# Kernel optimization log

Hardware: AMD Instinct MI355X
Metric: run time of the kernel (lower is better)

Reference implementation:

```python
import jax, jax.numpy as jnp
import numpy as np

T, N, F = 8, 4096, 256  # timesteps, nodes, feature dim (in=out for both layers)


def _uniform(key, shape, fan):
    s = 1.0 / np.sqrt(fan)
    return jax.random.uniform(key, shape, jnp.float32, -s, s)


def setup_inputs() -> dict:
    key = jax.random.key(0)
    ks = jax.random.split(key, 32)
    inp = {}
    # dense stand-in for the normalized sparse adjacency Ahat, per timestep
    inp["A"] = jax.random.normal(ks[0], (T, N, N), jnp.float32) * 0.01
    inp["X"] = jax.random.normal(ks[1], (T, N, F), jnp.float32)
    inp["mask"] = jnp.zeros((T, N), jnp.int32)  # only mask.shape[0] is used
    i = 2
    for l in range(2):
        inp[f"l{l}_scorer"] = _uniform(ks[i], (F, 1), F); i += 1
        for g in ("z", "r", "h"):
            inp[f"l{l}_W{g}"] = _uniform(ks[i], (F, F), F); i += 1
            inp[f"l{l}_U{g}"] = _uniform(ks[i], (F, F), F); i += 1
            inp[f"l{l}_b{g}"] = jnp.zeros((F, F), jnp.float32)
        inp[f"l{l}_Q0"] = _uniform(ks[i], (F, F), F); i += 1  # GCN_init_weights
    return inp


def _run_layer(A, Xseq, scorer, Wz, Uz, bz, Wr, Ur, br, Wh, Uh, bh, Q0):
    sn = jnp.linalg.norm(scorer)
    k = Q0.shape[1]  # cols = out_feats

    def step(Q, xs):
        Ahat, embs = xs  # [N,N], [N,F]
        # TopK module: scale rows by tanh(score), take first k rows, transpose -> [F, k]
        scores = (embs @ scorer) / sn            # [N,1]
        zt = (embs * jnp.tanh(scores))[:k].T     # [F, k]
        # matrix GRU evolving the GCN weight matrix Q [F, k]
        upd = jax.nn.sigmoid(Wz @ zt + Uz @ Q + bz)
        rst = jax.nn.sigmoid(Wr @ zt + Ur @ Q + br)
        hcap = jnp.tanh(Wh @ zt + Uh @ (rst * Q) + bh)
        Qn = (1.0 - upd) * Q + upd * hcap
        # GCN step: relu(Ahat @ (embs @ Qn))
        out = jax.nn.relu(Ahat @ (embs @ Qn))    # [N, k]
        return Qn, out

    _, outs = jax.lax.scan(step, Q0, (A, Xseq))
    return outs  # [T, N, k]


def reference(A, X, mask,
              l0_scorer, l0_Wz, l0_Uz, l0_bz, l0_Wr, l0_Ur, l0_br, l0_Wh, l0_Uh, l0_bh, l0_Q0,
              l1_scorer, l1_Wz, l1_Uz, l1_bz, l1_Wr, l1_Ur, l1_br, l1_Wh, l1_Uh, l1_bh, l1_Q0):
    h1 = _run_layer(A, X, l0_scorer, l0_Wz, l0_Uz, l0_bz, l0_Wr, l0_Ur, l0_br, l0_Wh, l0_Uh, l0_bh, l0_Q0)
    h2 = _run_layer(A, h1, l1_scorer, l1_Wz, l1_Uz, l1_bz, l1_Wr, l1_Ur, l1_br, l1_Wh, l1_Uh, l1_bh, l1_Q0)
    return h2[-1]  # [N, F] (skipfeats=False)
```

## Files before the change

kernel.cpp:

```cpp
#include <hip/hip_runtime.h>
#include <math.h>


typedef unsigned short u16;
typedef __attribute__((ext_vector_type(8))) short bhalf8;
typedef __attribute__((ext_vector_type(16))) float f32x16;

__device__ __forceinline__ void split2(float f, unsigned &h, unsigned &l){
  unsigned u = __float_as_uint(f);
  h = u >> 16;
  float r = f - __uint_as_float(u & 0xFFFF0000u);
  l = __float_as_uint(r) >> 16;
}

__launch_bounds__(256)
__global__ void prep_kernel(const float* __restrict__ q0, const float* __restrict__ q1,
                            const float* __restrict__ sc0, const float* __restrict__ sc1,
                            float* __restrict__ q0a, float* __restrict__ q1a,
                            float* __restrict__ sn){
  int b = blockIdx.x, tid = threadIdx.x;
  if (b < 256){ q0a[b*256 + tid] = q0[b*256 + tid]; }
  else if (b < 512){ int r = b - 256; q1a[r*256 + tid] = q1[r*256 + tid]; }
  else {
    __shared__ float s0[256], s1[256];
    float a = sc0[tid]; float c = sc1[tid];
    s0[tid] = a*a; s1[tid] = c*c; __syncthreads();
    for (int off = 128; off > 0; off >>= 1){
      if (tid < off){ s0[tid] += s0[tid+off]; s1[tid] += s1[tid+off]; }
      __syncthreads();
    }
    if (tid == 0){ sn[0] = sqrtf(s0[0]); sn[1] = sqrtf(s1[0]); }
  }
}

__launch_bounds__(256)
__global__ void scores_kernel(const float* __restrict__ emb, long embStrideT,
                              const float* __restrict__ scorer,
                              const float* __restrict__ sn, int snIdx,
                              float* __restrict__ ts, int tsStrideT){
  int t = blockIdx.y;
  int wave = threadIdx.x >> 6, lane = threadIdx.x & 63;
  int j = blockIdx.x*4 + wave;
  const float* row = emb + (long)t*embStrideT + (long)j*256;
  float s = 0.f;
  for (int c = lane; c < 256; c += 64) s += row[c] * scorer[c];
  for (int off = 32; off > 0; off >>= 1) s += __shfl_down(s, off);
  if (lane == 0) ts[t*tsStrideT + j] = tanhf(s / sn[snIdx]);
}

__launch_bounds__(256)
__global__ void split_kernel(const float* __restrict__ src, long sStride,
                             u16* __restrict__ dh, u16* __restrict__ dl,
                             long dStride, int n8){
  int z = blockIdx.y;
  const float* S = src + (long)z * sStride;
  u16* H = dh + (long)z * dStride;
  u16* L = dl + (long)z * dStride;
  int i = blockIdx.x * 256 + threadIdx.x;
  if (i >= n8) return;
  long o = (long)i * 8;
  float4 v0 = *(const float4*)(S + o);
  float4 v1 = *(const float4*)(S + o + 4);
  unsigned h0,h1,h2,h3,h4,h5,h6,h7, l0,l1,l2,l3,l4,l5,l6,l7;
  split2(v0.x,h0,l0); split2(v0.y,h1,l1); split2(v0.z,h2,l2); split2(v0.w,h3,l3);
  split2(v1.x,h4,l4); split2(v1.y,h5,l5); split2(v1.z,h6,l6); split2(v1.w,h7,l7);
  uint4 ph, pl;
  ph.x = h0 | (h1<<16); ph.y = h2 | (h3<<16); ph.z = h4 | (h5<<16); ph.w = h6 | (h7<<16);
  pl.x = l0 | (l1<<16); pl.y = l2 | (l3<<16); pl.z = l4 | (l5<<16); pl.w = l6 | (l7<<16);
  *(uint4*)(H + o) = ph;
  *(uint4*)(L + o) = pl;
}

__launch_bounds__(256)
__global__ void tconv_kernel(const float* __restrict__ src, long sStride,
                             u16* __restrict__ dh, u16* __restrict__ dl, long dStride){
  int z = blockIdx.z;
  const float* S = src + (long)z * sStride;
  u16* H = dh + (long)z * dStride;
  u16* L = dl + (long)z * dStride;
  int k0 = blockIdx.x << 5, n0 = blockIdx.y << 5;
  int c = threadIdx.x & 31, r = threadIdx.x >> 5;
  __shared__ float s[32][33];
  #pragma unroll
  for (int i = 0; i < 4; i++)
    s[r + 8*i][c] = S[(long)(k0 + r + 8*i) * 256 + n0 + c];
  __syncthreads();
  #pragma unroll
  for (int i = 0; i < 4; i++){
    int rr = r + 8*i;
    unsigned h, l;
    split2(s[c][rr], h, l);
    H[(long)(n0 + rr) * 4096 + k0 + c] = (u16)h;
    L[(long)(n0 + rr) * 4096 + k0 + c] = (u16)l;
  }
}

__device__ __forceinline__ int swzA(int row, int kb){
  return (row << 7) + (kb ^ ((row & 7) << 4));
}

__launch_bounds__(256, 2)
// ... 81 lines not shown
  float* po = pout + (long)(m0 + wm) * 256 + (n0 + wn);
  int rb16 = lhi << 2;
  #pragma unroll
  for (int reg = 0; reg < 16; reg++){
    int r = (reg & 3) + ((reg >> 2) << 3) + rb16;
    po[(long)r * 256 + ln31]              = acc00[reg];
    po[(long)r * 256 + 32 + ln31]         = acc01[reg];
    po[(long)(r + 32) * 256 + ln31]       = acc10[reg];
    po[(long)(r + 32) * 256 + 32 + ln31]  = acc11[reg];
  }
}

__launch_bounds__(256)
__global__ void reduce4_kernel(const float* __restrict__ P, long zStrideP, long ksStride,
                               float* __restrict__ out, long zStrideO, int count4, int relu){
  int z = blockIdx.y;
  const float* p = P + (long)z * zStrideP;
  float* o = out + (long)z * zStrideO;
  int i = blockIdx.x * 256 + threadIdx.x;
  if (i >= count4) return;
  long b = (long)i * 4;
  float4 v0 = *(const float4*)(p + b);
  float4 v1 = *(const float4*)(p + ksStride + b);
  float4 v2 = *(const float4*)(p + 2*ksStride + b);
  float4 v3 = *(const float4*)(p + 3*ksStride + b);
  float4 r;
  r.x = v0.x+v1.x+v2.x+v3.x; r.y = v0.y+v1.y+v2.y+v3.y;
  r.z = v0.z+v1.z+v2.z+v3.z; r.w = v0.w+v1.w+v2.w+v3.w;
  if (relu){ r.x=fmaxf(r.x,0.f); r.y=fmaxf(r.y,0.f); r.z=fmaxf(r.z,0.f); r.w=fmaxf(r.w,0.f); }
  *(float4*)(o + b) = r;
}

__launch_bounds__(256)
__global__ void gates_kernel(const float* __restrict__ emb,
                             const float* __restrict__ Wz, const float* __restrict__ Wr, const float* __restrict__ Wh,
                             const float* __restrict__ Uz, const float* __restrict__ Ur,
                             const float* __restrict__ bz, const float* __restrict__ br,
                             const float* __restrict__ Qcur, const float* __restrict__ ts,
                             float* __restrict__ G){
  int bx = blockIdx.x;
  int g = bx >> 6, tile = bx & 63;
  int m0 = (tile >> 3) << 5, j0 = (tile & 7) << 5;
  const float* W = (g==0) ? Wz : (g==1) ? Wr : Wh;
  int tid = threadIdx.x, tx = tid & 15, ty = tid >> 4;
  int rs = tid >> 3, cs = (tid & 7) << 2;
  __shared__ float sA[32][33];
  __shared__ float sB[32][33];
  float a00=0,a01=0,a10=0,a11=0;
  for (int k0 = 0; k0 < 256; k0 += 32){
    const float* pw = W   + (m0+rs)*256 + k0 + cs;
    const float* pe = emb + (long)(j0+rs)*256 + k0 + cs;
    sA[rs][cs+0]=pw[0]; sA[rs][cs+1]=pw[1]; sA[rs][cs+2]=pw[2]; sA[rs][cs+3]=pw[3];
    sB[cs+0][rs]=pe[0]; sB[cs+1][rs]=pe[1]; sB[cs+2][rs]=pe[2]; sB[cs+3][rs]=pe[3];
    __syncthreads();
    #pragma unroll
    for (int k = 0; k < 32; k++){
      float x0=sA[ty][k], x1=sA[ty+16][k], y0=sB[k][tx], y1=sB[k][tx+16];
      a00 += x0*y0; a01 += x0*y1; a10 += x1*y0; a11 += x1*y1;
    }
    __syncthreads();
  }
  float t0 = ts[j0+tx], t1 = ts[j0+tx+16];
  a00*=t0; a10*=t0; a01*=t1; a11*=t1;
  if (g == 2){
    G[2*65536 + (m0+ty   )*256 + j0+tx   ] = a00;
    G[2*65536 + (m0+ty   )*256 + j0+tx+16] = a01;
    G[2*65536 + (m0+ty+16)*256 + j0+tx   ] = a10;
    G[2*65536 + (m0+ty+16)*256 + j0+tx+16] = a11;
    return;
  }
  const float* U  = (g==0) ? Uz : Ur;
  const float* bb = (g==0) ? bz : br;
  float u00=0,u01=0,u10=0,u11=0;
  for (int k0 = 0; k0 < 256; k0 += 32){
    const float* pu = U    + (m0+rs)*256 + k0 + cs;
    const float* pq = Qcur + (k0+rs)*256 + j0 + cs;
    sA[rs][cs+0]=pu[0]; sA[rs][cs+1]=pu[1]; sA[rs][cs+2]=pu[2]; sA[rs][cs+3]=pu[3];
    sB[rs][cs+0]=pq[0]; sB[rs][cs+1]=pq[1]; sB[rs][cs+2]=pq[2]; sB[rs][cs+3]=pq[3];
    __syncthreads();
    #pragma unroll
    for (int k = 0; k < 32; k++){
      float x0=sA[ty][k], x1=sA[ty+16][k], y0=sB[k][tx], y1=sB[k][tx+16];
      u00 += x0*y0; u01 += x0*y1; u10 += x1*y0; u11 += x1*y1;
    }
    __syncthreads();
  }
  int m = m0+ty, j = j0+tx;
  float v;
  v = a00+u00+bb[m*256+j];          G[g*65536 + m*256+j]          = 1.f/(1.f+__expf(-v));
  v = a01+u01+bb[m*256+j+16];       G[g*65536 + m*256+j+16]       = 1.f/(1.f+__expf(-v));
  v = a10+u10+bb[(m+16)*256+j];     G[g*65536 + (m+16)*256+j]     = 1.f/(1.f+__expf(-v));
  v = a11+u11+bb[(m+16)*256+j+16];  G[g*65536 + (m+16)*256+j+16]  = 1.f/(1.f+__expf(-v));
}

__launch_bounds__(256)
__global__ void update_kernel(const float* __restrict__ Uh, const float* __restrict__ bh,
                              const float* __restrict__ G, const float* __restrict__ Qcur,
                              float* __restrict__ Qnew){
  int tile = blockIdx.x;
  int m0 = (tile >> 3) << 5, j0 = (tile & 7) << 5;
  int tid = threadIdx.x, tx = tid & 15, ty = tid >> 4;
  int rs = tid >> 3, cs = (tid & 7) << 2;
  __shared__ float sA[32][33];
  __shared__ float sB[32][33];
  float a00=0,a01=0,a10=0,a11=0;
  for (int k0 = 0; k0 < 256; k0 += 32){
    const float* pu = Uh + (m0+rs)*256 + k0 + cs;
    const float* pr = G + 65536 + (k0+rs)*256 + j0 + cs;
    const float* pq = Qcur      + (k0+rs)*256 + j0 + cs;
    sA[rs][cs+0]=pu[0]; sA[rs][cs+1]=pu[1]; sA[rs][cs+2]=pu[2]; sA[rs][cs+3]=pu[3];
    sB[rs][cs+0]=pr[0]*pq[0]; sB[rs][cs+1]=pr[1]*pq[1]; sB[rs][cs+2]=pr[2]*pq[2]; sB[rs][cs+3]=pr[3]*pq[3];
    __syncthreads();
    #pragma unroll
    for (int k = 0; k < 32; k++){
      float x0=sA[ty][k], x1=sA[ty+16][k], y0=sB[k][tx], y1=sB[k][tx+16];
      a00 += x0*y0; a01 += x0*y1; a10 += x1*y0; a11 += x1*y1;
    }
    __syncthreads();
  }
  #pragma unroll
  for (int ii = 0; ii < 2; ii++){
    #pragma unroll
    for (int jj = 0; jj < 2; jj++){
      float acc = (ii==0) ? (jj==0?a00:a01) : (jj==0?a10:a11);
      int m = m0 + ty + ii*16, j = j0 + tx + jj*16;
      float h = tanhf(acc + G[2*65536 + m*256 + j] + bh[m*256+j]);
      float z = G[m*256 + j];
      float q = Qcur[m*256 + j];
      Qnew[m*256 + j] = (1.f - z)*q + z*h;
    }
  }
}

__launch_bounds__(256)
__global__ void small_gemm_kernel(const float* __restrict__ Am, const float* __restrict__ Bm,
                                  float* __restrict__ C, int relu){
  int bx = blockIdx.x;
  int m0 = (bx >> 3) << 5, j0 = (bx & 7) << 5;
  int tid = threadIdx.x, tx = tid & 15, ty = tid >> 4;
  int rs = tid >> 3, cs = (tid & 7) << 2;
  __shared__ float sA[32][33];
  __shared__ float sB[32][33];
  float a00=0,a01=0,a10=0,a11=0;
  for (int k0 = 0; k0 < 256; k0 += 32){
    const float* pa = Am + (long)(m0+rs)*256 + k0 + cs;
    const float* pb = Bm + (long)(k0+rs)*256 + j0 + cs;
    sA[rs][cs+0]=pa[0]; sA[rs][cs+1]=pa[1]; sA[rs][cs+2]=pa[2]; sA[rs][cs+3]=pa[3];
    sB[rs][cs+0]=pb[0]; sB[rs][cs+1]=pb[1]; sB[rs][cs+2]=pb[2]; sB[rs][cs+3]=pb[3];
    __syncthreads();
    #pragma unroll
    for (int k = 0; k < 32; k++){
      float x0=sA[ty][k], x1=sA[ty+16][k], y0=sB[k][tx], y1=sB[k][tx+16];
      a00 += x0*y0; a01 += x0*y1; a10 += x1*y0; a11 += x1*y1;
    }
    __syncthreads();
  }
  if (relu){ a00=fmaxf(a00,0.f); a01=fmaxf(a01,0.f); a10=fmaxf(a10,0.f); a11=fmaxf(a11,0.f); }
  C[(long)(m0+ty   )*256 + j0+tx   ] = a00;
  C[(long)(m0+ty   )*256 + j0+tx+16] = a01;
  C[(long)(m0+ty+16)*256 + j0+tx   ] = a10;
  C[(long)(m0+ty+16)*256 + j0+tx+16] = a11;
}

extern "C" void kernel_launch(void* const* d_in, const int* in_sizes, int n_in,
                              void* d_out, int out_size, void* d_ws, size_t ws_size,
                              hipStream_t stream){
  (void)in_sizes; (void)n_in; (void)out_size; (void)ws_size;
  const int N = 4096, F = 256;

  const float* A = (const float*)d_in[0];
  const float* X = (const float*)d_in[1];
  const float *SC[2], *WZ[2], *UZ[2], *BZ[2], *WR[2], *UR[2], *BR[2], *WH[2], *UH[2], *BH[2], *Q0I[2];
  for (int l = 0; l < 2; l++){
    int b = 3 + l*11;
    SC[l]  = (const float*)d_in[b+0];
    WZ[l]  = (const float*)d_in[b+1];  UZ[l] = (const float*)d_in[b+2];  BZ[l] = (const float*)d_in[b+3];
    WR[l]  = (const float*)d_in[b+4];  UR[l] = (const float*)d_in[b+5];  BR[l] = (const float*)d_in[b+6];
    WH[l]  = (const float*)d_in[b+7];  UH[l] = (const float*)d_in[b+8];  BH[l] = (const float*)d_in[b+9];
    Q0I[l] = (const float*)d_in[b+10];
  }

  char* w = (char*)d_ws;
  float* sn   = (float*)(w);
  float* q0a  = (float*)(w + 1024);
  float* q0b  = q0a + 65536;
  float* q1a  = q0b + 65536;
  float* q1b  = q1a + 65536;
  float* ts0  = q1b + 65536;
  float* ts1  = ts0 + 2048;
  float* G    = ts1 + 256;
  float* Bmat = G + 3*65536;
  float* C7   = Bmat + 7*65536;
  float* H1   = C7 + 1048576;
  float* Z    = C7;
  u16* A7H = (u16*)(H1 + 1048576);
  u16* A7L = A7H + 16777216;
  u16* ArH = A7L + 16777216;
  u16* ArL = ArH + 7340032;
  u16* XtH = ArL + 7340032;
  u16* XtL = XtH + 8388608;
  u16* ZtH = XtL + 8388608;
  u16* ZtL = ZtH + 1048576;
  float* PB = (float*)(ZtL + 1048576);
  float* PC = PB + 1835008;

  prep_kernel<<<513, 256, 0, stream>>>(Q0I[0], Q0I[1], SC[0], SC[1], q0a, q1a, sn);
  scores_kernel<<<dim3(64, 8), 256, 0, stream>>>(X, (long)N*F, SC[0], sn, 0, ts0, 256);
  split_kernel<<<dim3(8192, 1), 256, 0, stream>>>(A + (long)7*N*N, 0, A7H, A7L, 0, 2097152);
  split_kernel<<<dim3(512, 7), 256, 0, stream>>>(A, (long)N*N, ArH, ArL, 1048576, 131072);
  tconv_kernel<<<dim3(128, 8, 8), 256, 0, stream>>>(X, 1048576, XtH, XtL, 1048576);
  gemm_mfma<<<dim3(2, 2, 28), 256, 0, stream>>>(ArH, ArL, 1048576, XtH, XtL, 1048576, PB, 262144);
  gemm_mfma<<<dim3(32, 2, 4), 256, 0, stream>>>(A7H, A7L, 0, XtH + 7*1048576, XtL + 7*1048576, 0, PC, 0);
  reduce4_kernel<<<dim3(64, 7), 256, 0, stream>>>(PB, 262144, 65536, Bmat, 65536, 16384, 0);
  reduce4_kernel<<<dim3(1024, 1), 256, 0, stream>>>(PC, 0, 1048576, C7, 0, 262144, 0);

  float *q0c = q0a, *q0n = q0b, *q1c = q1a, *q1n = q1b;
  for (int t = 0; t < 8; t++){
    gates_kernel<<<192, 256, 0, stream>>>(X + (long)t*N*F, WZ[0], WR[0], WH[0], UZ[0], UR[0],
                                          BZ[0], BR[0], q0c, ts0 + t*256, G);
    update_kernel<<<64, 256, 0, stream>>>(UH[0], BH[0], G, q0c, q0n);
    if (t < 7) small_gemm_kernel<<<64,   256, 0, stream>>>(Bmat + t*65536, q0n, H1, 1);
    else       small_gemm_kernel<<<1024, 256, 0, stream>>>(C7, q0n, H1, 1);
    scores_kernel<<<dim3(64, 1), 256, 0, stream>>>(H1, 0, SC[1], sn, 1, ts1, 0);
    gates_kernel<<<192, 256, 0, stream>>>(H1, WZ[1], WR[1], WH[1], UZ[1], UR[1],
                                          BZ[1], BR[1], q1c, ts1, G);
    update_kernel<<<64, 256, 0, stream>>>(UH[1], BH[1], G, q1c, q1n);
    float* tmp;
    tmp = q0c; q0c = q0n; q0n = tmp;
    tmp = q1c; q1c = q1n; q1n = tmp;
  }

  small_gemm_kernel<<<1024, 256, 0, stream>>>(H1, q1c, Z, 0);
  tconv_kernel<<<dim3(128, 8, 1), 256, 0, stream>>>(Z, 0, ZtH, ZtL, 0);
  gemm_mfma<<<dim3(32, 2, 4), 256, 0, stream>>>(A7H, A7L, 0, ZtH, ZtL, 0, PC, 0);
  reduce4_kernel<<<dim3(1024, 1), 256, 0, stream>>>(PC, 0, 1048576, (float*)d_out, 0, 262144, 1);
}
```

Baseline: 1.388 ms.

## Fuse per-timestep GRU loop into one persistent kernel with grid barriers and MFMA

```diff
diff --git a/kernel.cpp b/kernel.cpp
--- a/kernel.cpp
+++ b/kernel.cpp
@@ -13,24 +13,129 @@
   l = __float_as_uint(r) >> 16;
 }
 
+__device__ __forceinline__ int swz64(int row, int kb){
+  return (row << 7) + (kb ^ ((row & 7) << 4));
+}
+
+__device__ __forceinline__ bhalf8 frag(const u16* s, int row, int kb){
+  return *(const bhalf8*)((const char*)s + swz64(row, kb));
+}
+
+__device__ __forceinline__ f32x16 mm3(bhalf8 ah, bhalf8 al, bhalf8 bh, bhalf8 bl, f32x16 acc){
+  acc = __builtin_amdgcn_mfma_f32_32x32x16_bf16(ah, bh, acc, 0, 0, 0);
+  acc = __builtin_amdgcn_mfma_f32_32x32x16_bf16(ah, bl, acc, 0, 0, 0);
+  acc = __builtin_amdgcn_mfma_f32_32x32x16_bf16(al, bh, acc, 0, 0, 0);
+  return acc;
+}
+
+__device__ __forceinline__ void stage_f32s(const float* src, long ld, int rows, long k0,
+                                           const float* scale, u16* sH, u16* sL, int tid){
+  int rb = tid >> 2, ke = (tid & 3) << 4;
+  for (int r0 = 0; r0 < rows; r0 += 64){
+    int r = r0 + rb; if (r >= rows) break;
+    const float* p = src + (long)r*ld + k0 + ke;
+    float sc = scale ? scale[r] : 1.0f;
+    unsigned hh[16], ll[16];
+    #pragma unroll
+    for (int q = 0; q < 4; q++){
+      float4 v = *(const float4*)(p + q*4);
+      split2(v.x*sc, hh[q*4+0], ll[q*4+0]); split2(v.y*sc, hh[q*4+1], ll[q*4+1]);
+      split2(v.z*sc, hh[q*4+2], ll[q*4+2]); split2(v.w*sc, hh[q*4+3], ll[q*4+3]);
+    }
+    uint4 p0, p1, q0, q1;
+    p0.x = hh[0]|(hh[1]<<16);  p0.y = hh[2]|(hh[3]<<16);  p0.z = hh[4]|(hh[5]<<16);  p0.w = hh[6]|(hh[7]<<16);
+    p1.x = hh[8]|(hh[9]<<16);  p1.y = hh[10]|(hh[11]<<16);p1.z = hh[12]|(hh[13]<<16);p1.w = hh[14]|(hh[15]<<16);
+    q0.x = ll[0]|(ll[1]<<16);  q0.y = ll[2]|(ll[3]<<16);  q0.z = ll[4]|(ll[5]<<16);  q0.w = ll[6]|(ll[7]<<16);
+    q1.x = ll[8]|(ll[9]<<16);  q1.y = ll[10]|(ll[11]<<16);q1.z = ll[12]|(ll[13]<<16);q1.w = ll[14]|(ll[15]<<16);
+    int o0 = swz64(r, ke << 1), o1 = swz64(r, (ke << 1) + 16);
+    *(uint4*)((char*)sH + o0) = p0; *(uint4*)((char*)sH + o1) = p1;
+    *(uint4*)((char*)sL + o0) = q0; *(uint4*)((char*)sL + o1) = q1;
+  }
+}
+
+__device__ __forceinline__ void stage_cp(const u16* srcH, const u16* srcL, long ld, int rows,
+                                         long k0, u16* sH, u16* sL, int tid){
+  int rb = tid >> 2, ke = (tid & 3) << 4;
+  for (int r0 = 0; r0 < rows; r0 += 64){
+    int r = r0 + rb; if (r >= rows) break;
+    long g = (long)r*ld + k0 + ke;
+    uint4 a = *(const uint4*)(srcH + g), b = *(const uint4*)(srcH + g + 8);
+    uint4 c = *(const uint4*)(srcL + g), d = *(const uint4*)(srcL + g + 8);
+    int o0 = swz64(r, ke << 1), o1 = swz64(r, (ke << 1) + 16);
+    *(uint4*)((char*)sH + o0) = a; *(uint4*)((char*)sH + o1) = b;
+    *(uint4*)((char*)sL + o0) = c; *(uint4*)((char*)sL + o1) = d;
+  }
+}
+
+__device__ __forceinline__ void stage_prod(const float* a, const float* b, long ld, int rows,
+                                           long k0, u16* sH, u16* sL, int tid){
+  int rb = tid >> 2, ke = (tid & 3) << 4;
+  for (int r0 = 0; r0 < rows; r0 += 64){
+    int r = r0 + rb; if (r >= rows) break;
+    const float* pa = a + (long)r*ld + k0 + ke;
+    const float* pb = b + (long)r*ld + k0 + ke;
+    unsigned hh[16], ll[16];
+    #pragma unroll
+    for (int q = 0; q < 4; q++){
+      float4 va = *(const float4*)(pa + q*4);
+      float4 vb = *(const float4*)(pb + q*4);
+      split2(va.x*vb.x, hh[q*4+0], ll[q*4+0]); split2(va.y*vb.y, hh[q*4+1], ll[q*4+1]);
+      split2(va.z*vb.z, hh[q*4+2], ll[q*4+2]); split2(va.w*vb.w, hh[q*4+3], ll[q*4+3]);
+    }
+    uint4 p0, p1, q0, q1;
+    p0.x = hh[0]|(hh[1]<<16);  p0.y = hh[2]|(hh[3]<<16);  p0.z = hh[4]|(hh[5]<<16);  p0.w = hh[6]|(hh[7]<<16);
+    p1.x = hh[8]|(hh[9]<<16);  p1.y = hh[10]|(hh[11]<<16);p1.z = hh[12]|(hh[13]<<16);p1.w = hh[14]|(hh[15]<<16);
+    q0.x = ll[0]|(ll[1]<<16);  q0.y = ll[2]|(ll[3]<<16);  q0.z = ll[4]|(ll[5]<<16);  q0.w = ll[6]|(ll[7]<<16);
+    q1.x = ll[8]|(ll[9]<<16);  q1.y = ll[10]|(ll[11]<<16);q1.z = ll[12]|(ll[13]<<16);q1.w = ll[14]|(ll[15]<<16);
+    int o0 = swz64(r, ke << 1), o1 = swz64(r, (ke << 1) + 16);
+    *(uint4*)((char*)sH + o0) = p0; *(uint4*)((char*)sH + o1) = p1;
+    *(uint4*)((char*)sL + o0) = q0; *(uint4*)((char*)sL + o1) = q1;
+  }
+}
+
+__device__ __forceinline__ void twrite_f32(const float* ldsT, float* dst, int m0, int j0, int tid){
+  int jc = tid >> 2, seg = tid & 3;
+  float* p = dst + (long)(j0 + jc)*256 + m0 + (seg << 4);
+  #pragma unroll
+  for (int q = 0; q < 4; q++){
+    float4 o;
+    o.x = ldsT[(seg*16 + q*4 + 0)*65 + jc];
+    o.y = ldsT[(seg*16 + q*4 + 1)*65 + jc];
+    o.z = ldsT[(seg*16 + q*4 + 2)*65 + jc];
+    o.w = ldsT[(seg*16 + q*4 + 3)*65 + jc];
+    *(float4*)(p + q*4) = o;
+  }
+}
+
+__device__ __forceinline__ void twrite_bf16(const float* ldsT, u16* dh, u16* dl, int m0, int j0, int tid){
+  int jc = tid >> 2, seg = tid & 3;
+  unsigned hh[16], ll[16];
+  #pragma unroll
+  for (int q = 0; q < 16; q++)
+    split2(ldsT[(seg*16 + q)*65 + jc], hh[q], ll[q]);
+  uint4 p0, p1, q0, q1;
+  p0.x = hh[0]|(hh[1]<<16);  p0.y = hh[2]|(hh[3]<<16);  p0.z = hh[4]|(hh[5]<<16);  p0.w = hh[6]|(hh[7]<<16);
+  p1.x = hh[8]|(hh[9]<<16);  p1.y = hh[10]|(hh[11]<<16);p1.z = hh[12]|(hh[13]<<16);p1.w = hh[14]|(hh[15]<<16);
+  q0.x = ll[0]|(ll[1]<<16);  q0.y = ll[2]|(ll[3]<<16);  q0.z = ll[4]|(ll[5]<<16);  q0.w = ll[6]|(ll[7]<<16);
+  q1.x = ll[8]|(ll[9]<<16);  q1.y = ll[10]|(ll[11]<<16);q1.z = ll[12]|(ll[13]<<16);q1.w = ll[14]|(ll[15]<<16);
+  u16* ph = dh + (long)(j0 + jc)*256 + m0 + (seg << 4);
+  u16* pl = dl + (long)(j0 + jc)*256 + m0 + (seg << 4);
+  ((uint4*)ph)[0] = p0; ((uint4*)ph)[1] = p1;
+  ((uint4*)pl)[0] = q0; ((uint4*)pl)[1] = q1;
+}
+
 __launch_bounds__(256)
-__global__ void prep_kernel(const float* __restrict__ q0, const float* __restrict__ q1,
-                            const float* __restrict__ sc0, const float* __restrict__ sc1,
-                            float* __restrict__ q0a, float* __restrict__ q1a,
-                            float* __restrict__ sn){
-  int b = blockIdx.x, tid = threadIdx.x;
-  if (b < 256){ q0a[b*256 + tid] = q0[b*256 + tid]; }
-  else if (b < 512){ int r = b - 256; q1a[r*256 + tid] = q1[r*256 + tid]; }
-  else {
-    __shared__ float s0[256], s1[256];
-    float a = sc0[tid]; float c = sc1[tid];
-    s0[tid] = a*a; s1[tid] = c*c; __syncthreads();
-    for (int off = 128; off > 0; off >>= 1){
-      if (tid < off){ s0[tid] += s0[tid+off]; s1[tid] += s1[tid+off]; }
-      __syncthreads();
-    }
-    if (tid == 0){ sn[0] = sqrtf(s0[0]); sn[1] = sqrtf(s1[0]); }
-  }
+__global__ void norm_kernel(const float* __restrict__ sc0, const float* __restrict__ sc1,
+                            float* __restrict__ sn, int* __restrict__ bar){
+  int tid = threadIdx.x;
+  __shared__ float s0[256], s1[256];
+  float a = sc0[tid], c = sc1[tid];
+  s0[tid] = a*a; s1[tid] = c*c; __syncthreads();
+  for (int off = 128; off > 0; off >>= 1){
+    if (tid < off){ s0[tid] += s0[tid+off]; s1[tid] += s1[tid+off]; }
+    __syncthreads();
+  }
+  if (tid == 0){ sn[0] = sqrtf(s0[0]); sn[1] = sqrtf(s1[0]); *bar = 0; }
 }
 
 __launch_bounds__(256)
@@ -46,6 +151,58 @@
   for (int c = lane; c < 256; c += 64) s += row[c] * scorer[c];
   for (int off = 32; off > 0; off >>= 1) s += __shfl_down(s, off);
   if (lane == 0) ts[t*tsStrideT + j] = tanhf(s / sn[snIdx]);
+}
+
+__launch_bounds__(256)
+__global__ void prepq_kernel(const float* __restrict__ q0, const float* __restrict__ q1,
+                             float* __restrict__ Qf, float* __restrict__ QTf,
+                             u16* __restrict__ QTh, u16* __restrict__ QTl){
+  int l = blockIdx.y, tid = threadIdx.x;
+  const float* src = l ? q1 : q0;
+  long base = (long)l * 131072;
+  int bx = blockIdx.x, k0 = (bx >> 3) << 5, j0 = (bx & 7) << 5;
+  int c = tid & 31, r = tid >> 5;
+  __shared__ float s[32][33];
+  #pragma unroll
+  for (int i = 0; i < 4; i++){
+    int rr = r + 8*i;
+    float v = src[(k0+rr)*256 + j0+c];
+    s[rr][c] = v;
+    Qf[base + (long)(k0+rr)*256 + j0+c] = v;
+  }
+  __syncthreads();
+  #pragma unroll
+  for (int i = 0; i < 4; i++){
+    int rr = r + 8*i;
+    float v = s[c][rr];
+    long o = base + (long)(j0+rr)*256 + k0 + c;
+    QTf[o] = v;
+    unsigned h, lo; split2(v, h, lo);
+    QTh[o] = (u16)h; QTl[o] = (u16)lo;
+  }
+}
+
+__launch_bounds__(256)
+__global__ void split9_kernel(const float* m0,const float* m1,const float* m2,
+                              const float* m3,const float* m4,const float* m5,
+                              const float* m6,const float* m7,const float* m8,
+                              u16* __restrict__ SPL){
+  int z = blockIdx.y;
+  const float* src = (z==0)?m0:(z==1)?m1:(z==2)?m2:(z==3)?m3:(z==4)?m4:(z==5)?m5:(z==6)?m6:(z==7)?m7:m8;
+  u16* H = SPL + (long)z*131072;
+  u16* L = H + 65536;
+  int i = blockIdx.x*256 + threadIdx.x;
+  long o = (long)i * 8;
+  float4 v0 = *(const float4*)(src + o);
+  float4 v1 = *(const float4*)(src + o + 4);
+  unsigned h0,h1,h2,h3,h4,h5,h6,h7, l0,l1,l2,l3,l4,l5,l6,l7;
+  split2(v0.x,h0,l0); split2(v0.y,h1,l1); split2(v0.z,h2,l2); split2(v0.w,h3,l3);
+  split2(v1.x,h4,l4); split2(v1.y,h5,l5); split2(v1.z,h6,l6); split2(v1.w,h7,l7);
+  uint4 ph, pl;
+  ph.x = h0|(h1<<16); ph.y = h2|(h3<<16); ph.z = h4|(h5<<16); ph.w = h6|(h7<<16);
+  pl.x = l0|(l1<<16); pl.y = l2|(l3<<16); pl.z = l4|(l5<<16); pl.w = l6|(l7<<16);
+  *(uint4*)(H + o) = ph;
+  *(uint4*)(L + o) = pl;
 }
 
 __launch_bounds__(256)
@@ -65,8 +222,8 @@
   split2(v0.x,h0,l0); split2(v0.y,h1,l1); split2(v0.z,h2,l2); split2(v0.w,h3,l3);
   split2(v1.x,h4,l4); split2(v1.y,h5,l5); split2(v1.z,h6,l6); split2(v1.w,h7,l7);
   uint4 ph, pl;
-  ph.x = h0 | (h1<<16); ph.y = h2 | (h3<<16); ph.z = h4 | (h5<<16); ph.w = h6 | (h7<<16);
-  pl.x = l0 | (l1<<16); pl.y = l2 | (l3<<16); pl.z = l4 | (l5<<16); pl.w = l6 | (l7<<16);
+  ph.x = h0|(h1<<16); ph.y = h2|(h3<<16); ph.z = h4|(h5<<16); ph.w = h6|(h7<<16);
+  pl.x = l0|(l1<<16); pl.y = l2|(l3<<16); pl.z = l4|(l5<<16); pl.w = l6|(l7<<16);
   *(uint4*)(H + o) = ph;
   *(uint4*)(L + o) = pl;
 }
@@ -214,134 +371,375 @@
 }
 
 __launch_bounds__(256)
-__global__ void gates_kernel(const float* __restrict__ emb,
-                             const float* __restrict__ Wz, const float* __restrict__ Wr, const float* __restrict__ Wh,
-                             const float* __restrict__ Uz, const float* __restrict__ Ur,
-                             const float* __restrict__ bz, const float* __restrict__ br,
-                             const float* __restrict__ Qcur, const float* __restrict__ ts,
-                             float* __restrict__ G){
-  int bx = blockIdx.x;
-  int g = bx >> 6, tile = bx & 63;
-  int m0 = (tile >> 3) << 5, j0 = (tile & 7) << 5;
+__global__ void wg0_kernel(const float* __restrict__ Wz, const float* __restrict__ Wr,
+                           const float* __restrict__ Wh, const float* __restrict__ X,
+                           const float* __restrict__ ts0, float* __restrict__ WG0){
+  int tile = blockIdx.x, by = blockIdx.y;
+  int t = by / 3, g = by - t*3;
   const float* W = (g==0) ? Wz : (g==1) ? Wr : Wh;
-  int tid = threadIdx.x, tx = tid & 15, ty = tid >> 4;
-  int rs = tid >> 3, cs = (tid & 7) << 2;
-  __shared__ float sA[32][33];
-  __shared__ float sB[32][33];
-  float a00=0,a01=0,a10=0,a11=0;
-  for (int k0 = 0; k0 < 256; k0 += 32){
-    const float* pw = W   + (m0+rs)*256 + k0 + cs;
-    const float* pe = emb + (long)(j0+rs)*256 + k0 + cs;
-    sA[rs][cs+0]=pw[0]; sA[rs][cs+1]=pw[1]; sA[rs][cs+2]=pw[2]; sA[rs][cs+3]=pw[3];
-    sB[cs+0][rs]=pe[0]; sB[cs+1][rs]=pe[1]; sB[cs+2][rs]=pe[2]; sB[cs+3][rs]=pe[3];
-    __syncthreads();
-    #pragma unroll
-    for (int k = 0; k < 32; k++){
-      float x0=sA[ty][k], x1=sA[ty+16][k], y0=sB[k][tx], y1=sB[k][tx+16];
-      a00 += x0*y0; a01 += x0*y1; a10 += x1*y0; a11 += x1*y1;
-    }
-    __syncthreads();
-  }
-  float t0 = ts[j0+tx], t1 = ts[j0+tx+16];
-  a00*=t0; a10*=t0; a01*=t1; a11*=t1;
-  if (g == 2){
-    G[2*65536 + (m0+ty   )*256 + j0+tx   ] = a00;
-    G[2*65536 + (m0+ty   )*256 + j0+tx+16] = a01;
-    G[2*65536 + (m0+ty+16)*256 + j0+tx   ] = a10;
-    G[2*65536 + (m0+ty+16)*256 + j0+tx+16] = a11;
-    return;
-  }
-  const float* U  = (g==0) ? Uz : Ur;
-  const float* bb = (g==0) ? bz : br;
-  float u00=0,u01=0,u10=0,u11=0;
-  for (int k0 = 0; k0 < 256; k0 += 32){
-    const float* pu = U    + (m0+rs)*256 + k0 + cs;
-    const float* pq = Qcur + (k0+rs)*256 + j0 + cs;
-    sA[rs][cs+0]=pu[0]; sA[rs][cs+1]=pu[1]; sA[rs][cs+2]=pu[2]; sA[rs][cs+3]=pu[3];
-    sB[rs][cs+0]=pq[0]; sB[rs][cs+1]=pq[1]; sB[rs][cs+2]=pq[2]; sB[rs][cs+3]=pq[3];
-    __syncthreads();
-    #pragma unroll
-    for (int k = 0; k < 32; k++){
-      float x0=sA[ty][k], x1=sA[ty+16][k], y0=sB[k][tx], y1=sB[k][tx+16];
-      u00 += x0*y0; u01 += x0*y1; u10 += x1*y0; u11 += x1*y1;
-    }
-    __syncthreads();
-  }
-  int m = m0+ty, j = j0+tx;
-  float v;
-  v = a00+u00+bb[m*256+j];          G[g*65536 + m*256+j]          = 1.f/(1.f+__expf(-v));
-  v = a01+u01+bb[m*256+j+16];       G[g*65536 + m*256+j+16]       = 1.f/(1.f+__expf(-v));
-  v = a10+u10+bb[(m+16)*256+j];     G[g*65536 + (m+16)*256+j]     = 1.f/(1.f+__expf(-v));
-  v = a11+u11+bb[(m+16)*256+j+16];  G[g*65536 + (m+16)*256+j+16]  = 1.f/(1.f+__expf(-v));
-}
-
-__launch_bounds__(256)
-__global__ void update_kernel(const float* __restrict__ Uh, const float* __restrict__ bh,
-                              const float* __restrict__ G, const float* __restrict__ Qcur,
-                              float* __restrict__ Qnew){
-  int tile = blockIdx.x;
-  int m0 = (tile >> 3) << 5, j0 = (tile & 7) << 5;
-  int tid = threadIdx.x, tx = tid & 15, ty = tid >> 4;
-  int rs = tid >> 3, cs = (tid & 7) << 2;
-  __shared__ float sA[32][33];
-  __shared__ float sB[32][33];
-  float a00=0,a01=0,a10=0,a11=0;
-  for (int k0 = 0; k0 < 256; k0 += 32){
-    const float* pu = Uh + (m0+rs)*256 + k0 + cs;
-    const float* pr = G + 65536 + (k0+rs)*256 + j0 + cs;
-    const float* pq = Qcur      + (k0+rs)*256 + j0 + cs;
-    sA[rs][cs+0]=pu[0]; sA[rs][cs+1]=pu[1]; sA[rs][cs+2]=pu[2]; sA[rs][cs+3]=pu[3];
-    sB[rs][cs+0]=pr[0]*pq[0]; sB[rs][cs+1]=pr[1]*pq[1]; sB[rs][cs+2]=pr[2]*pq[2]; sB[rs][cs+3]=pr[3]*pq[3];
-    __syncthreads();
-    #pragma unroll
-    for (int k = 0; k < 32; k++){
-      float x0=sA[ty][k], x1=sA[ty+16][k], y0=sB[k][tx], y1=sB[k][tx+16];
-      a00 += x0*y0; a01 += x0*y1; a10 += x1*y0; a11 += x1*y1;
-    }
-    __syncthreads();
-  }
-  #pragma unroll
-  for (int ii = 0; ii < 2; ii++){
-    #pragma unroll
-    for (int jj = 0; jj < 2; jj++){
-      float acc = (ii==0) ? (jj==0?a00:a01) : (jj==0?a10:a11);
-      int m = m0 + ty + ii*16, j = j0 + tx + jj*16;
-      float h = tanhf(acc + G[2*65536 + m*256 + j] + bh[m*256+j]);
-      float z = G[m*256 + j];
-      float q = Qcur[m*256 + j];
-      Qnew[m*256 + j] = (1.f - z)*q + z*h;
-    }
-  }
-}
-
-__launch_bounds__(256)
-__global__ void small_gemm_kernel(const float* __restrict__ Am, const float* __restrict__ Bm,
-                                  float* __restrict__ C, int relu){
-  int bx = blockIdx.x;
-  int m0 = (bx >> 3) << 5, j0 = (bx & 7) << 5;
-  int tid = threadIdx.x, tx = tid & 15, ty = tid >> 4;
-  int rs = tid >> 3, cs = (tid & 7) << 2;
-  __shared__ float sA[32][33];
-  __shared__ float sB[32][33];
-  float a00=0,a01=0,a10=0,a11=0;
-  for (int k0 = 0; k0 < 256; k0 += 32){
-    const float* pa = Am + (long)(m0+rs)*256 + k0 + cs;
-    const float* pb = Bm + (long)(k0+rs)*256 + j0 + cs;
-    sA[rs][cs+0]=pa[0]; sA[rs][cs+1]=pa[1]; sA[rs][cs+2]=pa[2]; sA[rs][cs+3]=pa[3];
-    sB[rs][cs+0]=pb[0]; sB[rs][cs+1]=pb[1]; sB[rs][cs+2]=pb[2]; sB[rs][cs+3]=pb[3];
-    __syncthreads();
-    #pragma unroll
-    for (int k = 0; k < 32; k++){
-      float x0=sA[ty][k], x1=sA[ty+16][k], y0=sB[k][tx], y1=sB[k][tx+16];
-      a00 += x0*y0; a01 += x0*y1; a10 += x1*y0; a11 += x1*y1;
-    }
-    __syncthreads();
-  }
-  if (relu){ a00=fmaxf(a00,0.f); a01=fmaxf(a01,0.f); a10=fmaxf(a10,0.f); a11=fmaxf(a11,0.f); }
-  C[(long)(m0+ty   )*256 + j0+tx   ] = a00;
-  C[(long)(m0+ty   )*256 + j0+tx+16] = a01;
-  C[(long)(m0+ty+16)*256 + j0+tx   ] = a10;
-  C[(long)(m0+ty+16)*256 + j0+tx+16] = a11;
+  const float* Xt = X + (long)t * 1048576;
+  int m0 = (tile >> 2) << 6, j0 = (tile & 3) << 6;
+  int tid = threadIdx.x, lane = tid & 63, wave = tid >> 6;
+  int ln31 = lane & 31, lhi = lane >> 5;
+  int wm = (wave >> 1) << 5, wn = (wave & 1) << 5;
+  __shared__ __align__(16) char LDSw[32768];
+  u16* sAh = (u16*)LDSw;          u16* sAl = (u16*)(LDSw + 8192);
+  u16* sBh = (u16*)(LDSw + 16384); u16* sBl = (u16*)(LDSw + 24576);
+  f32x16 acc;
+  #pragma unroll
+  for (int i = 0; i < 16; i++) acc[i] = 0.f;
+  for (int kk = 0; kk < 4; kk++){
+    long k0 = (long)kk << 6;
+    stage_f32s(W + (long)m0*256, 256, 64, k0, nullptr, sAh, sAl, tid);
+    stage_f32s(Xt + (long)j0*256, 256, 64, k0, ts0 + t*256 + j0, sBh, sBl, tid);
+    __syncthreads();
+    #pragma unroll
+    for (int s = 0; s < 4; s++){
+      int kb = (s << 5) + (lhi << 4);
+      acc = mm3(frag(sAh, wm+ln31, kb), frag(sAl, wm+ln31, kb),
+                frag(sBh, wn+ln31, kb), frag(sBl, wn+ln31, kb), acc);
+    }
+    __syncthreads();
+  }
+  float* o = WG0 + (long)by * 65536;
+  int rb = lhi << 2;
+  #pragma unroll
+  for (int reg = 0; reg < 16; reg++){
+    int r = (reg & 3) + ((reg >> 2) << 3) + rb;
+    o[(long)(m0 + wm + r)*256 + j0 + wn + ln31] = acc[reg];
+  }
+}
+
+__launch_bounds__(256, 2)
+__global__ void gemm_k256(const float* __restrict__ A,
+                          const u16* __restrict__ Bh, const u16* __restrict__ Bl,
+                          float* __restrict__ Cout, u16* __restrict__ TH, u16* __restrict__ TL,
+                          long ldT, int mode){
+  int m0 = blockIdx.x << 7, n0 = blockIdx.y << 7;
+  int tid = threadIdx.x, lane = tid & 63, wave = tid >> 6;
+  int ln31 = lane & 31, lhi = lane >> 5;
+  int wm = (wave >> 1) << 6, wn = (wave & 1) << 6;
+  __shared__ __align__(16) char LDSg[66560];
+  u16* sAh = (u16*)LDSg;            u16* sAl = (u16*)(LDSg + 16384);
+  u16* sBh = (u16*)(LDSg + 32768);  u16* sBl = (u16*)(LDSg + 49152);
+  f32x16 acc00, acc01, acc10, acc11;
+  #pragma unroll
+  for (int i = 0; i < 16; i++){ acc00[i]=0.f; acc01[i]=0.f; acc10[i]=0.f; acc11[i]=0.f; }
+  for (int kk = 0; kk < 4; kk++){
+    long k0 = (long)kk << 6;
+    stage_f32s(A + (long)m0*256, 256, 128, k0, nullptr, sAh, sAl, tid);
+    stage_cp(Bh + (long)n0*256, Bl + (long)n0*256, 256, 128, k0, sBh, sBl, tid);
+    __syncthreads();
+    #pragma unroll
+    for (int s = 0; s < 4; s++){
+      int kb = (s << 5) + (lhi << 4);
+      bhalf8 a0h = frag(sAh, wm+ln31, kb),    a0l = frag(sAl, wm+ln31, kb);
+      bhalf8 a1h = frag(sAh, wm+32+ln31, kb), a1l = frag(sAl, wm+32+ln31, kb);
+      bhalf8 b0h = frag(sBh, wn+ln31, kb),    b0l = frag(sBl, wn+ln31, kb);
+      bhalf8 b1h = frag(sBh, wn+32+ln31, kb), b1l = frag(sBl, wn+32+ln31, kb);
+      acc00 = mm3(a0h, a0l, b0h, b0l, acc00);
+      acc01 = mm3(a0h, a0l, b1h, b1l, acc01);
+      acc10 = mm3(a1h, a1l, b0h, b0l, acc10);
+      acc11 = mm3(a1h, a1l, b1h, b1l, acc11);
+    }
+    __syncthreads();
+  }
+  int rb = lhi << 2;
+  if (mode == 0){
+    float* o = Cout + (long)(m0 + wm)*256 + n0 + wn;
+    #pragma unroll
+    for (int reg = 0; reg < 16; reg++){
+      int r = (reg & 3) + ((reg >> 2) << 3) + rb;
+      o[(long)r*256 + ln31]             = fmaxf(acc00[reg], 0.f);
+      o[(long)r*256 + 32 + ln31]        = fmaxf(acc01[reg], 0.f);
+      o[(long)(r+32)*256 + ln31]        = fmaxf(acc10[reg], 0.f);
+      o[(long)(r+32)*256 + 32 + ln31]   = fmaxf(acc11[reg], 0.f);
+    }
+  } else {
+    float* ldsT = (float*)LDSg;
+    #pragma unroll
+    for (int reg = 0; reg < 16; reg++){
+      int r = (reg & 3) + ((reg >> 2) << 3) + rb;
+      ldsT[(wm + r)*129 + wn + ln31]           = acc00[reg];
+      ldsT[(wm + r)*129 + wn + 32 + ln31]      = acc01[reg];
+      ldsT[(wm + 32 + r)*129 + wn + ln31]      = acc10[reg];
+      ldsT[(wm + 32 + r)*129 + wn + 32 + ln31] = acc11[reg];
+    }
+    __syncthreads();
+    int nl = tid >> 1, seg = tid & 1;
+    u16* ph = TH + (long)(n0 + nl)*ldT + m0 + (seg << 6);
+    u16* pl = TL + (long)(n0 + nl)*ldT + m0 + (seg << 6);
+    #pragma unroll
+    for (int q = 0; q < 8; q++){
+      unsigned hh[8], ll[8];
+      #pragma unroll
+      for (int j = 0; j < 8; j++)
+        split2(ldsT[(seg*64 + q*8 + j)*129 + nl], hh[j], ll[j]);
+      uint4 vh, vl;
+      vh.x = hh[0]|(hh[1]<<16); vh.y = hh[2]|(hh[3]<<16); vh.z = hh[4]|(hh[5]<<16); vh.w = hh[6]|(hh[7]<<16);
+      vl.x = ll[0]|(ll[1]<<16); vl.y = ll[2]|(ll[3]<<16); vl.z = ll[4]|(ll[5]<<16); vl.w = ll[6]|(ll[7]<<16);
+      ((uint4*)ph)[q] = vh;
+      ((uint4*)pl)[q] = vl;
+    }
+  }
+}
+
+__device__ __forceinline__ void gbar(int* bar, int target){
+  __syncthreads();
+  if (threadIdx.x == 0){
+    __threadfence();
+    atomicAdd(bar, 1);
+    while (__hip_atomic_load(bar, __ATOMIC_ACQUIRE, __HIP_MEMORY_SCOPE_AGENT) < target)
+      __builtin_amdgcn_s_sleep(1);
+    __threadfence();
+  }
+  __syncthreads();
+}
+
+__device__ void phase_gates(int g, int tile,
+    const u16* WH_, const u16* WL_, const float* H1_, const float* ts1_,
+    const u16* UH_, const u16* UL_, const u16* QTH_, const u16* QTL_,
+    const float* addmat, const float* bias,
+    float* zout, float* rTout, float* hwout, char* LDSp, int tid)
+{
+  int m0 = (tile >> 2) << 6, j0 = (tile & 3) << 6;
+  u16* sA1h = (u16*)LDSp;             u16* sA1l = (u16*)(LDSp + 8192);
+  u16* sB1h = (u16*)(LDSp + 16384);   u16* sB1l = (u16*)(LDSp + 24576);
+  u16* sA2h = (u16*)(LDSp + 32768);   u16* sA2l = (u16*)(LDSp + 40960);
+  u16* sB2h = (u16*)(LDSp + 49152);   u16* sB2l = (u16*)(LDSp + 57344);
+  int lane = tid & 63, wave = tid >> 6;
+  int ln31 = lane & 31, lhi = lane >> 5;
+  int wm = (wave >> 1) << 5, wn = (wave & 1) << 5;
+  bool doU = (g < 2);
+  f32x16 acc;
+  #pragma unroll
+  for (int i = 0; i < 16; i++) acc[i] = 0.f;
+  for (int kk = 0; kk < 4; kk++){
+    long k0 = (long)kk << 6;
+    if (WH_){
+      stage_cp(WH_ + (long)m0*256, WL_ + (long)m0*256, 256, 64, k0, sA1h, sA1l, tid);
+      stage_f32s(H1_ + (long)j0*256, 256, 64, k0, ts1_ + j0, sB1h, sB1l, tid);
+    }
+    if (doU){
+      stage_cp(UH_ + (long)m0*256, UL_ + (long)m0*256, 256, 64, k0, sA2h, sA2l, tid);
+      stage_cp(QTH_ + (long)j0*256, QTL_ + (long)j0*256, 256, 64, k0, sB2h, sB2l, tid);
+    }
+    __syncthreads();
+    #pragma unroll
+    for (int s = 0; s < 4; s++){
+      int kb = (s << 5) + (lhi << 4);
+      if (WH_)
+        acc = mm3(frag(sA1h, wm+ln31, kb), frag(sA1l, wm+ln31, kb),
+                  frag(sB1h, wn+ln31, kb), frag(sB1l, wn+ln31, kb), acc);
+      if (doU)
+        acc = mm3(frag(sA2h, wm+ln31, kb), frag(sA2l, wm+ln31, kb),
+                  frag(sB2h, wn+ln31, kb), frag(sB2l, wn+ln31, kb), acc);
+    }
+    __syncthreads();
+  }
+  int rb = lhi << 2;
+  if (g == 0){
+    #pragma unroll
+    for (int reg = 0; reg < 16; reg++){
+      int r = (reg & 3) + ((reg >> 2) << 3) + rb;
+      int gm = m0 + wm + r, gj = j0 + wn + ln31;
+      float v = acc[reg];
+      if (addmat) v += addmat[gm*256 + gj];
+      v += bias[gm*256 + gj];
+      zout[gm*256 + gj] = 1.f/(1.f + __expf(-v));
+    }
+  } else if (g == 1){
+    float* ldsT = (float*)LDSp;
+    #pragma unroll
+    for (int reg = 0; reg < 16; reg++){
+      int r = (reg & 3) + ((reg >> 2) << 3) + rb;
+      int gm = m0 + wm + r, gj = j0 + wn + ln31;
+      float v = acc[reg];
+      if (addmat) v += addmat[gm*256 + gj];
+      v += bias[gm*256 + gj];
+      ldsT[(wm + r)*65 + wn + ln31] = 1.f/(1.f + __expf(-v));
+    }
+    __syncthreads();
+    twrite_f32(ldsT, rTout, m0, j0, tid);
+  } else {
+    #pragma unroll
+    for (int reg = 0; reg < 16; reg++){
+      int r = (reg & 3) + ((reg >> 2) << 3) + rb;
+      int gm = m0 + wm + r, gj = j0 + wn + ln31;
+      hwout[gm*256 + gj] = acc[reg];
+    }
+  }
+}
+
+__device__ void phase_update(int tile, const u16* UHh, const u16* UHl,
+    const float* rT, const float* zb, const float* QTfC, const float* QfC,
+    const float* HW, const float* bh,
+    float* QfN, float* QTfN, u16* QThN, u16* QTlN, char* LDSp, int tid)
+{
+  int m0 = (tile >> 2) << 6, j0 = (tile & 3) << 6;
+  u16* sAh = (u16*)LDSp;            u16* sAl = (u16*)(LDSp + 8192);
+  u16* sBh = (u16*)(LDSp + 16384);  u16* sBl = (u16*)(LDSp + 24576);
+  int lane = tid & 63, wave = tid >> 6;
+  int ln31 = lane & 31, lhi = lane >> 5;
+  int wm = (wave >> 1) << 5, wn = (wave & 1) << 5;
+  f32x16 acc;
+  #pragma unroll
+  for (int i = 0; i < 16; i++) acc[i] = 0.f;
+  for (int kk = 0; kk < 4; kk++){
+    long k0 = (long)kk << 6;
+    stage_cp(UHh + (long)m0*256, UHl + (long)m0*256, 256, 64, k0, sAh, sAl, tid);
+    stage_prod(rT + (long)j0*256, QTfC + (long)j0*256, 256, 64, k0, sBh, sBl, tid);
+    __syncthreads();
+    #pragma unroll
+    for (int s = 0; s < 4; s++){
+      int kb = (s << 5) + (lhi << 4);
+      acc = mm3(frag(sAh, wm+ln31, kb), frag(sAl, wm+ln31, kb),
+                frag(sBh, wn+ln31, kb), frag(sBl, wn+ln31, kb), acc);
+    }
+    __syncthreads();
+  }
+  float* ldsT = (float*)LDSp;
+  int rb = lhi << 2;
+  #pragma unroll
+  for (int reg = 0; reg < 16; reg++){
+    int r = (reg & 3) + ((reg >> 2) << 3) + rb;
+    int gm = m0 + wm + r, gj = j0 + wn + ln31;
+    float hc = tanhf(acc[reg] + HW[gm*256 + gj] + bh[gm*256 + gj]);
+    float z  = zb[gm*256 + gj];
+    float qc = QfC[gm*256 + gj];
+    float qn = (1.f - z)*qc + z*hc;
+    QfN[gm*256 + gj] = qn;
+    ldsT[(wm + r)*65 + wn + ln31] = qn;
+  }
+  __syncthreads();
+  twrite_f32(ldsT, QTfN, m0, j0, tid);
+  twrite_bf16(ldsT, QThN, QTlN, m0, j0, tid);
+}
+
+__device__ void phase_C(int blk8, const float* Asrc,
+    const u16* QTh_, const u16* QTl_, const float* sc1, const float* sn,
+    float* H1, float* ts1, char* LDSp, int tid)
+{
+  int m0 = blk8 << 5;
+  u16* sBh = (u16*)LDSp;
+  u16* sBl = (u16*)(LDSp + 32768);
+  u16* sAh = (u16*)(LDSp + 65536);
+  u16* sAl = (u16*)(LDSp + 69632);
+  float* part = (float*)(LDSp + 73728);
+  int lane = tid & 63, wave = tid >> 6;
+  int ln31 = lane & 31, lhi = lane >> 5;
+  int wnc = wave << 6;
+  f32x16 a0, a1;
+  #pragma unroll
+  for (int i = 0; i < 16; i++){ a0[i]=0.f; a1[i]=0.f; }
+  for (int kk = 0; kk < 4; kk++){
+    long k0 = (long)kk << 6;
+    stage_f32s(Asrc + (long)m0*256, 256, 32, k0, nullptr, sAh, sAl, tid);
+    stage_cp(QTh_, QTl_, 256, 256, k0, sBh, sBl, tid);
+    __syncthreads();
+    #pragma unroll
+    for (int s = 0; s < 4; s++){
+      int kb = (s << 5) + (lhi << 4);
+      bhalf8 ah = frag(sAh, ln31, kb), al = frag(sAl, ln31, kb);
+      a0 = mm3(ah, al, frag(sBh, wnc+ln31, kb),    frag(sBl, wnc+ln31, kb),    a0);
+      a1 = mm3(ah, al, frag(sBh, wnc+32+ln31, kb), frag(sBl, wnc+32+ln31, kb), a1);
+    }
+    __syncthreads();
+  }
+  int rb = lhi << 2;
+  float s0 = sc1[wnc + ln31], s1 = sc1[wnc + 32 + ln31];
+  #pragma unroll
+  for (int reg = 0; reg < 16; reg++){
+    int r = (reg & 3) + ((reg >> 2) << 3) + rb;
+    float v0 = fmaxf(a0[reg], 0.f), v1 = fmaxf(a1[reg], 0.f);
+    H1[(long)(m0 + r)*256 + wnc + ln31]      = v0;
+    H1[(long)(m0 + r)*256 + wnc + 32 + ln31] = v1;
+    float c = v0*s0 + v1*s1;
+    c += __shfl_xor(c, 1);  c += __shfl_xor(c, 2);  c += __shfl_xor(c, 4);
+    c += __shfl_xor(c, 8);  c += __shfl_xor(c, 16);
+    if (ln31 == 0) part[wave*32 + r] = c;
+  }
+  __syncthreads();
+  if (tid < 32){
+    float s = part[tid] + part[32 + tid] + part[64 + tid] + part[96 + tid];
+    ts1[m0 + tid] = tanhf(s / sn[1]);
+  }
+}
+
+__launch_bounds__(256, 1)
+__global__ void scan_kernel(
+    float* __restrict__ Qf, float* __restrict__ QTf,
+    u16* __restrict__ QTh, u16* __restrict__ QTl,
+    const u16* __restrict__ SPL, const float* __restrict__ WG0,
+    float* __restrict__ zb0, float* __restrict__ rT0,
+    float* __restrict__ zb1, float* __restrict__ rT1,
+    float* __restrict__ HW1, float* __restrict__ H1, float* __restrict__ ts1,
+    const float* __restrict__ Bmat, const float* __restrict__ C7,
+    const float* __restrict__ bz0, const float* __restrict__ br0, const float* __restrict__ bh0,
+    const float* __restrict__ bz1, const float* __restrict__ br1, const float* __restrict__ bh1,
+    const float* __restrict__ sc1, const float* __restrict__ sn,
+    int* __restrict__ bar)
+{
+  __shared__ __align__(16) char LDS[81920];
+  int blk = blockIdx.x, tid = threadIdx.x;
+  int round = 0;
+
+  if (blk < 32){
+    int g = blk >> 4, tile = blk & 15;
+    phase_gates(g, tile, nullptr, nullptr, nullptr, nullptr,
+                SPL + (long)g*131072, SPL + (long)g*131072 + 65536,
+                QTh, QTl,
+                WG0 + (long)g*65536,
+                (g==0) ? bz0 : br0,
+                zb0, rT0, nullptr, LDS, tid);
+  }
+  gbar(bar, (++round) << 6);
+
+  for (int t = 0; t < 8; t++){
+    int cur = t & 1, nxt = cur ^ 1;
+    long q0c = (long)cur*65536,          q0n = (long)nxt*65536;
+    long q1c = 131072 + (long)cur*65536, q1n = 131072 + (long)nxt*65536;
+
+    if (blk < 16)
+      phase_update(blk, SPL + 2L*131072, SPL + 2L*131072 + 65536,
+                   rT0, zb0, QTf + q0c, Qf + q0c,
+                   WG0 + (long)(t*3 + 2)*65536, bh0,
+                   Qf + q0n, QTf + q0n, QTh + q0n, QTl + q0n, LDS, tid);
+    gbar(bar, (++round) << 6);
+
+    if (blk < 8)
+      phase_C(blk, (t < 7) ? (Bmat + (long)t*65536) : C7,
+              QTh + q0n, QTl + q0n, sc1, sn, H1, ts1, LDS, tid);
+    gbar(bar, (++round) << 6);
+
+    if (blk < 48){
+      int g = blk >> 4, tile = blk & 15;
+      phase_gates(g, tile,
+                  SPL + (long)(3+g)*131072, SPL + (long)(3+g)*131072 + 65536, H1, ts1,
+                  SPL + (long)(6+g)*131072, SPL + (long)(6+g)*131072 + 65536,
+                  QTh + q1c, QTl + q1c,
+                  nullptr,
+                  (g==0) ? bz1 : (g==1) ? br1 : nullptr,
+                  zb1, rT1, HW1, LDS, tid);
+    }
+    gbar(bar, (++round) << 6);
+
+    if (blk < 16)
+      phase_update(blk, SPL + 8L*131072, SPL + 8L*131072 + 65536,
+                   rT1, zb1, QTf + q1c, Qf + q1c,
+                   HW1, bh1,
+                   Qf + q1n, QTf + q1n, QTh + q1n, QTl + q1n, LDS, tid);
+    else if (blk < 48 && t < 7){
+      int bb = blk - 16, g = bb >> 4, tile = bb & 15;
+      phase_gates(g, tile, nullptr, nullptr, nullptr, nullptr,
+                  SPL + (long)g*131072, SPL + (long)g*131072 + 65536,
+                  QTh + q0n, QTl + q0n,
+                  WG0 + (long)((t+1)*3 + g)*65536,
+                  (g==0) ? bz0 : br0,
+                  zb0, rT0, nullptr, LDS, tid);
+    }
+    gbar(bar, (++round) << 6);
+  }
 }
 
 extern "C" void kernel_launch(void* const* d_in, const int* in_sizes, int n_in,
@@ -363,31 +761,42 @@
   }
 
   char* w = (char*)d_ws;
-  float* sn   = (float*)(w);
-  float* q0a  = (float*)(w + 1024);
-  float* q0b  = q0a + 65536;
-  float* q1a  = q0b + 65536;
-  float* q1b  = q1a + 65536;
-  float* ts0  = q1b + 65536;
+  float* sn   = (float*)w;
+  int*   bar  = (int*)(w + 64);
+  float* ts0  = (float*)(w + 1024);
   float* ts1  = ts0 + 2048;
-  float* G    = ts1 + 256;
-  float* Bmat = G + 3*65536;
-  float* C7   = Bmat + 7*65536;
-  float* H1   = C7 + 1048576;
-  float* Z    = C7;
-  u16* A7H = (u16*)(H1 + 1048576);
+  float* Qf   = ts1 + 256;
+  float* QTf  = Qf + 262144;
+  u16*   QTh  = (u16*)(QTf + 262144);
+  u16*   QTl  = QTh + 262144;
+  float* zb0  = (float*)(QTl + 262144);
+  float* rT0  = zb0 + 65536;
+  float* zb1  = rT0 + 65536;
+  float* rT1  = zb1 + 65536;
+  float* HW1  = rT1 + 65536;
+  float* H1s  = HW1 + 65536;
+  float* WG0  = H1s + 65536;
+  u16*   SPL  = (u16*)(WG0 + 1572864);
+  float* Bmat = (float*)(SPL + 1179648);
+  float* C7   = Bmat + 458752;
+  float* H1f  = C7 + 1048576;
+  u16* A7H = (u16*)(H1f + 1048576);
   u16* A7L = A7H + 16777216;
   u16* ArH = A7L + 16777216;
   u16* ArL = ArH + 7340032;
   u16* XtH = ArL + 7340032;
   u16* XtL = XtH + 8388608;
-  u16* ZtH = XtL + 8388608;
-  u16* ZtL = ZtH + 1048576;
-  float* PB = (float*)(ZtL + 1048576);
+  u16* ZTh = XtL + 8388608;
+  u16* ZTl = ZTh + 1048576;
+  float* PB = (float*)(ZTl + 1048576);
   float* PC = PB + 1835008;
 
-  prep_kernel<<<513, 256, 0, stream>>>(Q0I[0], Q0I[1], SC[0], SC[1], q0a, q1a, sn);
+  norm_kernel<<<1, 256, 0, stream>>>(SC[0], SC[1], sn, bar);
   scores_kernel<<<dim3(64, 8), 256, 0, stream>>>(X, (long)N*F, SC[0], sn, 0, ts0, 256);
+  prepq_kernel<<<dim3(64, 2), 256, 0, stream>>>(Q0I[0], Q0I[1], Qf, QTf, QTh, QTl);
+  split9_kernel<<<dim3(32, 9), 256, 0, stream>>>(UZ[0], UR[0], UH[0],
+                                                 WZ[1], WR[1], WH[1],
+                                                 UZ[1], UR[1], UH[1], SPL);
   split_kernel<<<dim3(8192, 1), 256, 0, stream>>>(A + (long)7*N*N, 0, A7H, A7L, 0, 2097152);
   split_kernel<<<dim3(512, 7), 256, 0, stream>>>(A, (long)N*N, ArH, ArL, 1048576, 131072);
   tconv_kernel<<<dim3(128, 8, 8), 256, 0, stream>>>(X, 1048576, XtH, XtL, 1048576);
@@ -395,25 +804,17 @@
   gemm_mfma<<<dim3(32, 2, 4), 256, 0, stream>>>(A7H, A7L, 0, XtH + 7*1048576, XtL + 7*1048576, 0, PC, 0);
   reduce4_kernel<<<dim3(64, 7), 256, 0, stream>>>(PB, 262144, 65536, Bmat, 65536, 16384, 0);
   reduce4_kernel<<<dim3(1024, 1), 256, 0, stream>>>(PC, 0, 1048576, C7, 0, 262144, 0);
-
-  float *q0c = q0a, *q0n = q0b, *q1c = q1a, *q1n = q1b;
-  for (int t = 0; t < 8; t++){
-    gates_kernel<<<192, 256, 0, stream>>>(X + (long)t*N*F, WZ[0], WR[0], WH[0], UZ[0], UR[0],
-                                          BZ[0], BR[0], q0c, ts0 + t*256, G);
-    update_kernel<<<64, 256, 0, stream>>>(UH[0], BH[0], G, q0c, q0n);
-    if (t < 7) small_gemm_kernel<<<64,   256, 0, stream>>>(Bmat + t*65536, q0n, H1, 1);
-    else       small_gemm_kernel<<<1024, 256, 0, stream>>>(C7, q0n, H1, 1);
-    scores_kernel<<<dim3(64, 1), 256, 0, stream>>>(H1, 0, SC[1], sn, 1, ts1, 0);
-    gates_kernel<<<192, 256, 0, stream>>>(H1, WZ[1], WR[1], WH[1], UZ[1], UR[1],
-                                          BZ[1], BR[1], q1c, ts1, G);
-    update_kernel<<<64, 256, 0, stream>>>(UH[1], BH[1], G, q1c, q1n);
-    float* tmp;
-    tmp = q0c; q0c = q0n; q0n = tmp;
-    tmp = q1c; q1c = q1n; q1n = tmp;
-  }
-
-  small_gemm_kernel<<<1024, 256, 0, stream>>>(H1, q1c, Z, 0);
-  tconv_kernel<<<dim3(128, 8, 1), 256, 0, stream>>>(Z, 0, ZtH, ZtL, 0);
-  gemm_mfma<<<dim3(32, 2, 4), 256, 0, stream>>>(A7H, A7L, 0, ZtH, ZtL, 0, PC, 0);
+  wg0_kernel<<<dim3(16, 24), 256, 0, stream>>>(WZ[0], WR[0], WH[0], X, ts0, WG0);
+
+  scan_kernel<<<64, 256, 0, stream>>>(Qf, QTf, QTh, QTl, SPL, WG0,
+                                      zb0, rT0, zb1, rT1, HW1, H1s, ts1,
+                                      Bmat, C7,
+                                      BZ[0], BR[0], BH[0], BZ[1], BR[1], BH[1],
+                                      SC[1], sn, bar);
+
+  gemm_k256<<<dim3(32, 2), 256, 0, stream>>>(C7, QTh, QTl, H1f, nullptr, nullptr, 0, 0);
+  gemm_k256<<<dim3(32, 2), 256, 0, stream>>>(H1f, QTh + 131072, QTl + 131072,
+                                             nullptr, ZTh, ZTl, 4096, 1);
+  gemm_mfma<<<dim3(32, 2, 4), 256, 0, stream>>>(A7H, A7L, 0, ZTh, ZTl, 0, PC, 0);
   reduce4_kernel<<<dim3(1024, 1), 256, 0, stream>>>(PC, 0, 1048576, (float*)d_out, 0, 262144, 1);
 }
```

After: 1.680 ms. +21.0%, slower.
